# Performance work log

Measured on AMD Instinct MI355X. Metric: run time of the kernel, lower is better.

The kernel has to match this reference:

```python
import jax, jax.numpy as jnp
import numpy as np

D = 256      # embed_dims
NH = 8       # num_heads
NL = 1       # num_levels
NP = 6       # num_points
BS = 1
NQ = 40000   # 200x200 BEV queries
H0, W0 = 200, 200
HD = D // NH


def _ln(x, g, b):
    m = jnp.mean(x, -1, keepdims=True)
    v = jnp.var(x, -1, keepdims=True)
    return (x - m) / jnp.sqrt(v + 1e-5) * g + b


def _bilinear(v, lx, ly, H, W):
    # v: (bs, h, H*W, hd); lx/ly: (bs, h, S) pixel coords (align_corners=False, zero padding)
    x0 = jnp.floor(lx).astype(jnp.int32)
    y0 = jnp.floor(ly).astype(jnp.int32)
    acc = 0.
    for dx in (0, 1):
        for dy in (0, 1):
            xi = x0 + dx
            yi = y0 + dy
            w = (1. - jnp.abs(lx - xi)) * (1. - jnp.abs(ly - yi))
            valid = (xi >= 0) & (xi < W) & (yi >= 0) & (yi < H)
            idx = jnp.clip(yi, 0, H - 1) * W + jnp.clip(xi, 0, W - 1)
            g = jnp.take_along_axis(v, idx[..., None], axis=2)  # (bs,h,S,hd)
            acc = acc + g * (w * valid)[..., None]
    return acc


def _forward(query, value, reference_points, W_off, b_off, W_attn, b_attn,
             W_val, b_val, W_out, b_out, ln1_g, ln1_b, W1, b1, W2, b2,
             ln2_g, ln2_b, ss, lsi):
    bs, nq, d = query.shape
    # sampling offsets and attention weights from the query
    off = (query @ W_off + b_off).reshape(bs, nq, NH, NL, NP, 2)
    attn = jax.nn.softmax((query @ W_attn + b_attn).reshape(bs, nq, NH, NL * NP), -1)
    attn = attn.reshape(bs, nq, NH, NL, NP)
    v = (value @ W_val + b_val).reshape(bs, -1, NH, HD).transpose(0, 2, 1, 3)  # (bs,h,HW,hd)
    # offset normalizer is [W, H] per level
    norm = jnp.stack([ss[:, 1], ss[:, 0]], -1).astype(query.dtype)  # (NL,2)
    loc = reference_points[:, :, None, :, None, :] + off / norm[None, None, None, :, None, :]
    out = jnp.zeros((bs, NH, nq, HD), query.dtype)
    for l in range(NL):
        Hl = int(ss[l, 0]); Wl = int(ss[l, 1]); st = int(lsi[l])
        vl = v[:, :, st:st + Hl * Wl]
        lx = (loc[:, :, :, l, :, 0] * Wl - 0.5).transpose(0, 2, 1, 3).reshape(bs, NH, nq * NP)
        ly = (loc[:, :, :, l, :, 1] * Hl - 0.5).transpose(0, 2, 1, 3).reshape(bs, NH, nq * NP)
        sampled = _bilinear(vl, lx, ly, Hl, Wl).reshape(bs, NH, nq, NP, HD)
        wl = attn[:, :, :, l, :].transpose(0, 2, 1, 3)  # (bs,h,nq,P)
        out = out + jnp.einsum('bhqp,bhqpd->bhqd', wl, sampled)
    y_msda = out.transpose(0, 2, 1, 3).reshape(bs, nq, d) @ W_out + b_out
    y = _ln(y_msda + query, ln1_g, ln1_b)
    y_ffn = jax.nn.gelu(y @ W1 + b1, approximate=False) @ W2 + b2
    return _ln(y_ffn + y, ln2_g, ln2_b)


def setup_inputs():
    key = jax.random.key(0)
    ks = jax.random.split(key, 12)
    s = 0.02
    return {
        'query': jax.random.normal(ks[0], (BS, NQ, D), jnp.float32),
        'value': jax.random.normal(ks[1], (BS, H0 * W0, D), jnp.float32),
        'reference_points': jax.random.uniform(ks[2], (BS, NQ, NL, 2), jnp.float32),
        'spatial_shapes': jnp.array([[H0, W0]], jnp.int32),
        'level_start_index': jnp.array([0], jnp.int32),
        'W_off': jax.random.normal(ks[3], (D, NH * NL * NP * 2), jnp.float32) * s,
        'b_off': jax.random.uniform(ks[4], (NH * NL * NP * 2,), jnp.float32, -1., 1.),
        'W_attn': jax.random.normal(ks[5], (D, NH * NL * NP), jnp.float32) * s,
        'b_attn': jnp.zeros((NH * NL * NP,), jnp.float32),
        'W_val': jax.random.normal(ks[6], (D, D), jnp.float32) * s,
        'b_val': jnp.zeros((D,), jnp.float32),
        'W_out': jax.random.normal(ks[7], (D, D), jnp.float32) * s,
        'b_out': jnp.zeros((D,), jnp.float32),
        'ln1_g': jnp.ones((D,), jnp.float32),
        'ln1_b': jnp.zeros((D,), jnp.float32),
        'W1': jax.random.normal(ks[8], (D, D), jnp.float32) * s,
        'b1': jnp.zeros((D,), jnp.float32),
        'W2': jax.random.normal(ks[9], (D, D), jnp.float32) * s,
        'b2': jnp.zeros((D,), jnp.float32),
        'ln2_g': jnp.ones((D,), jnp.float32),
        'ln2_b': jnp.zeros((D,), jnp.float32),
    }


def reference(query, value, reference_points, spatial_shapes, level_start_index,
              W_off, b_off, W_attn, b_attn, W_val, b_val, W_out, b_out,
              ln1_g, ln1_b, W1, b1, W2, b2, ln2_g, ln2_b):
    ss = np.asarray(spatial_shapes)
    lsi = np.asarray(level_start_index)
    return _forward(query, value, reference_points, W_off, b_off, W_attn, b_attn,
                    W_val, b_val, W_out, b_out, ln1_g, ln1_b, W1, b1, W2, b2,
                    ln2_g, ln2_b, ss, lsi)
```

## Files before the change

kernel.cpp:

```cpp
#include <hip/hip_runtime.h>
#include <math.h>

#define NQ 40000
#define DIM 256
#define NH 8
#define NP 6
#define HD 32
#define GH 200
#define GW 200
#define TS 8
#define TNX 25
#define NT 625

typedef short bf16x8 __attribute__((ext_vector_type(8)));
typedef float f32x4 __attribute__((ext_vector_type(4)));

__device__ __forceinline__ unsigned short f2bf(float f) {
    unsigned int u = __builtin_bit_cast(unsigned int, f);
    u += 0x7fffu + ((u >> 16) & 1u);
    return (unsigned short)(u >> 16);
}
__device__ __forceinline__ float bf2f(unsigned short h) {
    return __builtin_bit_cast(float, ((unsigned int)h) << 16);
}

__global__ void __launch_bounds__(256)
f2b_kernel(const float* __restrict__ q, unsigned short* __restrict__ qd,
           const float* __restrict__ v, unsigned short* __restrict__ vd) {
    int b = blockIdx.x;
    const float* src; unsigned short* dst;
    if (b < 5000) { src = q; dst = qd; } else { src = v; dst = vd; b -= 5000; }
    const int i = b * 256 + threadIdx.x;
    const float4* s = (const float4*)src;
    float4 a = s[(size_t)i * 2], c = s[(size_t)i * 2 + 1];
    bf16x8 o;
    o[0] = (short)f2bf(a.x); o[1] = (short)f2bf(a.y);
    o[2] = (short)f2bf(a.z); o[3] = (short)f2bf(a.w);
    o[4] = (short)f2bf(c.x); o[5] = (short)f2bf(c.y);
    o[6] = (short)f2bf(c.z); o[7] = (short)f2bf(c.w);
    *(bf16x8*)(dst + (size_t)i * 8) = o;
}

__global__ void __launch_bounds__(256)
wtrans_kernel(const float* __restrict__ Wval, const float* __restrict__ Woff,
              const float* __restrict__ Wattn, const float* __restrict__ Wout,
              const float* __restrict__ W1, const float* __restrict__ W2,
              const float* __restrict__ b_off, const float* __restrict__ b_attn,
              unsigned short* __restrict__ Bt, float* __restrict__ bias_oa) {
    __shared__ float T[64][65];
    const int m = blockIdx.z;
    const float* src; int N; int dr0;
    if (m == 0)      { src = Wval;  N = 256; dr0 = 0; }
    else if (m == 1) { src = Woff;  N = 96;  dr0 = 256; }
    else if (m == 2) { src = Wattn; N = 48;  dr0 = 352; }
    else if (m == 3) { src = Wout;  N = 256; dr0 = 400; }
    else if (m == 4) { src = W1;    N = 256; dr0 = 656; }
    else             { src = W2;    N = 256; dr0 = 912; }

    if (m == 1 && blockIdx.x == 0 && blockIdx.y == 0 && threadIdx.x < 144)
        bias_oa[threadIdx.x] = threadIdx.x < 96 ? b_off[threadIdx.x]
                                                : b_attn[threadIdx.x - 96];

    const int n0 = blockIdx.x * 64, k0 = blockIdx.y * 64;
    if (n0 >= N) return;
    const int col = threadIdx.x & 63, rg = threadIdx.x >> 6;
#pragma unroll
    for (int i = 0; i < 16; ++i) {
        const int r = rg + 4 * i;
        T[r][col] = (n0 + col < N) ? src[(size_t)(k0 + r) * N + n0 + col] : 0.0f;
    }
    __syncthreads();
#pragma unroll
    for (int i = 0; i < 16; ++i) {
        const int nl = rg + 4 * i;
        if (n0 + nl < N)
            Bt[(size_t)(dr0 + n0 + nl) * 256 + k0 + col] = f2bf(T[col][nl]);
    }
}

__device__ __forceinline__ int tile_of(const float* rp, int q) {
    const float rx = rp[q * 2 + 0] * (float)GW;
    const float ry = rp[q * 2 + 1] * (float)GH;
    const int tx = min(max((int)(rx * (1.0f / TS)), 0), TNX - 1);
    const int ty = min(max((int)(ry * (1.0f / TS)), 0), TNX - 1);
    return ty * TNX + tx;
}

__global__ void __launch_bounds__(256)
sort_zero(int* __restrict__ hist) {
    const int i = blockIdx.x * 256 + threadIdx.x;
    if (i < NT) hist[i] = 0;
}

__global__ void __launch_bounds__(256)
sort_hist(const float* __restrict__ rp, int* __restrict__ hist) {
    const int q = blockIdx.x * 256 + threadIdx.x;
    if (q >= NQ) return;
    atomicAdd(&hist[tile_of(rp, q)], 1);
}

__global__ void __launch_bounds__(64)
sort_scan(const int* __restrict__ hist, int* __restrict__ cursor) {
    const int lane = threadIdx.x;
    int loc[10]; int t = 0;
#pragma unroll
    for (int j = 0; j < 10; ++j) {
        const int idx = lane * 10 + j;
        loc[j] = t;
        t += (idx < NT) ? hist[idx] : 0;
    }
    int s = t;
#pragma unroll
    for (int o = 1; o < 64; o <<= 1) {
        const int u = __shfl_up(s, o);
        if (lane >= o) s += u;
    }
    const int ex = s - t;
#pragma unroll
    for (int j = 0; j < 10; ++j) {
        const int idx = lane * 10 + j;
        if (idx < NT) cursor[idx] = ex + loc[j];
    }
}

__global__ void __launch_bounds__(256)
sort_scatter(const float* __restrict__ rp, int* __restrict__ cursor,
             int* __restrict__ perm) {
    const int q = blockIdx.x * 256 + threadIdx.x;
    if (q >= NQ) return;
    const int pos = atomicAdd(&cursor[tile_of(rp, q)], 1);
    perm[pos] = q;
}

template <int EPI>
__global__ void __launch_bounds__(256)
gemm64(const unsigned short* __restrict__ A, const unsigned short* __restrict__ Bt,
       const float* __restrict__ bias, const void* __restrict__ res,
       const float* __restrict__ lng, const float* __restrict__ lnb,
       void* __restrict__ C, int M) {
    __shared__ __align__(16) unsigned short As[2][64 * 32];
    __shared__ __align__(16) unsigned short Bs[2][256 * 32];
    __shared__ __align__(16) float red[64][4][2];

    const int tid = threadIdx.x, lane = tid & 63, wave = tid >> 6;
    const int quad = lane >> 4, l16 = lane & 15;
    const int bm0 = blockIdx.x * 64;
    const int r16 = lane >> 2;
    const int ch = (lane & 3) * 8;

    f32x4 acc[4][4] = {};

    auto stage = [&](int kt, int buf) {
        const int k0 = kt * 32;
        {
            const int row = wave * 16 + r16;
            const unsigned short* gp = A + (size_t)(bm0 + row) * 256 + k0 + ch;
            __builtin_amdgcn_global_load_lds(
                (const __attribute__((address_space(1))) void*)gp,
                (__attribute__((address_space(3))) void*)(&As[buf][wave * 16 * 32]),
                16, 0, 0);
        }
#pragma unroll
        for (int j = 0; j < 4; ++j) {
            const int rowbase = (wave * 4 + j) * 16;
            const unsigned short* gp = Bt + (size_t)(rowbase + r16) * 256 + k0 + ch;
            __builtin_amdgcn_global_load_lds(
                (const __attribute__((address_space(1))) void*)gp,
                (__attribute__((address_space(3))) void*)(&Bs[buf][rowbase * 32]),
                16, 0, 0);
        }
    };

    stage(0, 0);
    __syncthreads();

    for (int kt = 0; kt < 8; ++kt) {
        const int cur = kt & 1;
        if (kt < 7) stage(kt + 1, 1 - cur);

        bf16x8 af[4], bw[4];
#pragma unroll
        for (int t = 0; t < 4; ++t) {
            af[t] = *(const bf16x8*)&As[cur][(t * 16 + l16) * 32 + quad * 8];
            bw[t] = *(const bf16x8*)&Bs[cur][(wave * 64 + t * 16 + l16) * 32 + quad * 8];
        }
#pragma unroll
        for (int tm = 0; tm < 4; ++tm)
#pragma unroll
            for (int tn = 0; tn < 4; ++tn)
                acc[tm][tn] = __builtin_amdgcn_mfma_f32_16x16x32_bf16(
                    af[tm], bw[tn], acc[tm][tn], 0, 0, 0);
        __syncthreads();
    }

    float bias4[4];
#pragma unroll
    for (int tn = 0; tn < 4; ++tn) bias4[tn] = bias[wave * 64 + tn * 16 + l16];

    if (EPI == 1 || EPI == 2) {
#pragma unroll
        for (int tm = 0; tm < 4; ++tm) {
            const int row0 = bm0 + tm * 16 + quad * 4;
#pragma unroll
            for (int tn = 0; tn < 4; ++tn) {
                const int col = wave * 64 + tn * 16 + l16;
#pragma unroll
                for (int r = 0; r < 4; ++r) {
                    float x = acc[tm][tn][r] + bias4[tn];
                    if (EPI == 1) x = 0.5f * x * (1.0f + erff(x * 0.70710678118654752f));
                    ((unsigned short*)C)[(size_t)(row0 + r) * 256 + col] = f2bf(x);
                }
            }
        }
        return;
    }

#pragma unroll
    for (int tm = 0; tm < 4; ++tm) {
#pragma unroll
        for (int r = 0; r < 4; ++r) {
            const size_t rb = (size_t)(bm0 + tm * 16 + quad * 4 + r) * 256;
#pragma unroll
            for (int tn = 0; tn < 4; ++tn) {
                const int col = wave * 64 + tn * 16 + l16;
                float e = acc[tm][tn][r] + bias4[tn];
                if (EPI == 3) e += ((const float*)res)[rb + col];
                else          e += bf2f(((const unsigned short*)res)[rb + col]);
                acc[tm][tn][r] = e;
            }
        }
    }
#pragma unroll
    for (int tm = 0; tm < 4; ++tm) {
#pragma unroll
        for (int r = 0; r < 4; ++r) {
            float s = 0.0f, sq = 0.0f;
#pragma unroll
            for (int tn = 0; tn < 4; ++tn) {
                const float e = acc[tm][tn][r];
                s += e; sq += e * e;
            }
#pragma unroll
            for (int o = 1; o < 16; o <<= 1) {
                s += __shfl_xor(s, o);
                sq += __shfl_xor(sq, o);
            }
            if (l16 == 0) {
                const int row = tm * 16 + quad * 4 + r;
                red[row][wave][0] = s;
                red[row][wave][1] = sq;
            }
        }
    }
    __syncthreads();

    float gv[4], bvv[4];
#pragma unroll
    for (int tn = 0; tn < 4; ++tn) {
        const int col = wave * 64 + tn * 16 + l16;
        gv[tn] = lng[col];
        bvv[tn] = lnb[col];
    }
#pragma unroll
    for (int tm = 0; tm < 4; ++tm) {
#pragma unroll
        for (int r = 0; r < 4; ++r) {
            const int row = tm * 16 + quad * 4 + r;
            const float4 p0 = *(const float4*)&red[row][0][0];
            const float4 p1 = *(const float4*)&red[row][2][0];
            const float sum = p0.x + p0.z + p1.x + p1.z;
            const float sumsq = p0.y + p0.w + p1.y + p1.w;
            const float mean = sum * (1.0f / 256.0f);
            const float var = sumsq * (1.0f / 256.0f) - mean * mean;
            const float rstd = rsqrtf(var + 1e-5f);
            const size_t rb = (size_t)(bm0 + row) * 256;
#pragma unroll
            for (int tn = 0; tn < 4; ++tn) {
                const int col = wave * 64 + tn * 16 + l16;
                const float o = (acc[tm][tn][r] - mean) * rstd * gv[tn] + bvv[tn];
                if (EPI == 3) ((unsigned short*)C)[rb + col] = f2bf(o);
                else          ((float*)C)[rb + col] = o;
            }
        }
    }
}

__global__ void __launch_bounds__(256)
gemm_bt(const unsigned short* __restrict__ A, const unsigned short* __restrict__ Bt,
        const float* __restrict__ bias, unsigned short* __restrict__ C,
        int M, int N, int ldc) {
    __shared__ __align__(16) unsigned short As[128 * 32];
    __shared__ __align__(16) unsigned short Bs[128 * 32];

    const int tid = threadIdx.x, lane = tid & 63, wave = tid >> 6;
    const int quad = lane >> 4, l16 = lane & 15;
    const int wm = wave >> 1, wn = wave & 1;
    const int bm0 = blockIdx.y * 128, bn0 = blockIdx.x * 128;

    f32x4 acc[4][4] = {};
    const int rl = lane >> 2;
    const int c8 = (lane & 3) * 8;

    for (int kt = 0; kt < 8; ++kt) {
        const int k0 = kt * 32;
        __syncthreads();
#pragma unroll
        for (int i = 0; i < 2; ++i) {
            const int rgrp = i * 64 + wave * 16;
            const int gA = min(bm0 + rgrp + rl, M - 1);
            const unsigned short* gpa = A + (size_t)gA * 256 + k0 + c8;
            __builtin_amdgcn_global_load_lds(
                (const __attribute__((address_space(1))) void*)gpa,
                (__attribute__((address_space(3))) void*)(As + (size_t)rgrp * 32),
                16, 0, 0);
            const int gB = min(bn0 + rgrp + rl, N - 1);
            const unsigned short* gpb = Bt + (size_t)gB * 256 + k0 + c8;
            __builtin_amdgcn_global_load_lds(
                (const __attribute__((address_space(1))) void*)gpb,
                (__attribute__((address_space(3))) void*)(Bs + (size_t)rgrp * 32),
                16, 0, 0);
        }
        __syncthreads();

        bf16x8 af[4], bw[4];
#pragma unroll
        for (int t = 0; t < 4; ++t) {
            af[t] = *(const bf16x8*)&As[(wm * 64 + t * 16 + l16) * 32 + quad * 8];
            bw[t] = *(const bf16x8*)&Bs[(wn * 64 + t * 16 + l16) * 32 + quad * 8];
        }
#pragma unroll
        for (int tm = 0; tm < 4; ++tm)
#pragma unroll
            for (int tn = 0; tn < 4; ++tn)
                acc[tm][tn] = __builtin_amdgcn_mfma_f32_16x16x32_bf16(
                    af[tm], bw[tn], acc[tm][tn], 0, 0, 0);
    }

#pragma unroll
    for (int tm = 0; tm < 4; ++tm) {
        const int row0 = bm0 + wm * 64 + tm * 16 + quad * 4;
#pragma unroll
        for (int tn = 0; tn < 4; ++tn) {
            const int col = bn0 + wn * 64 + tn * 16 + l16;
            if (col < N) {
                const float bv = bias[col];
#pragma unroll
                for (int r = 0; r < 4; ++r) {
                    const int row = row0 + r;
                    if (row < M)
                        C[(size_t)row * ldc + col] = f2bf(acc[tm][tn][r] + bv);
                }
            }
        }
    }
}

__global__ void __launch_bounds__(256)
msda_sample(const unsigned short* __restrict__ v,
            const unsigned short* __restrict__ oa,
            const float* __restrict__ rp,
            const int* __restrict__ perm,
            unsigned short* __restrict__ out) {
    const int b = blockIdx.x;
    const int w = (b & 7) * 625 + (b >> 3);
    const int tid = threadIdx.x;
    const int slot = tid >> 2;
    const int q = perm[w * 8 + (slot >> 3)];
    const int h = slot & 7;
    const int c0 = (tid & 3) * 8;

    const float rx = rp[q * 2 + 0] * (float)GW;
    const float ry = rp[q * 2 + 1] * (float)GH;

    const unsigned short* oaq = oa + (size_t)q * 144;
    float lg[NP];
    float mx = -1e30f;
#pragma unroll
    for (int p = 0; p < NP; ++p) {
        lg[p] = bf2f(oaq[96 + h * NP + p]);
        mx = fmaxf(mx, lg[p]);
    }
    float s = 0.0f;
#pragma unroll
    for (int p = 0; p < NP; ++p) { lg[p] = expf(lg[p] - mx); s += lg[p]; }
    const float inv = 1.0f / s;

    float acc[8] = {};
#pragma unroll
    for (int p = 0; p < NP; ++p) {
        const float aw = lg[p] * inv;
        const float lx = rx + bf2f(oaq[h * 12 + p * 2 + 0]) - 0.5f;
        const float ly = ry + bf2f(oaq[h * 12 + p * 2 + 1]) - 0.5f;
        const float fx0 = floorf(lx), fy0 = floorf(ly);
        const int x0 = (int)fx0, y0 = (int)fy0;
        const float fx = lx - fx0, fy = ly - fy0;
#pragma unroll
        for (int dy = 0; dy < 2; ++dy) {
            const int yi = y0 + dy;
            const float wyv = dy ? fy : 1.0f - fy;
#pragma unroll
            for (int dx = 0; dx < 2; ++dx) {
                const int xi = x0 + dx;
                const float wxv = dx ? fx : 1.0f - fx;
                const bool valid = (xi >= 0) & (xi < GW) & (yi >= 0) & (yi < GH);
                const int yc = min(max(yi, 0), GH - 1);
                const int xc = min(max(xi, 0), GW - 1);
                const float wgt = valid ? aw * wxv * wyv : 0.0f;
                const bf16x8 g = *(const bf16x8*)&v[((size_t)(yc * GW + xc)) * 256 + h * 32 + c0];
#pragma unroll
                for (int j = 0; j < 8; ++j)
                    acc[j] += bf2f((unsigned short)g[j]) * wgt;
            }
        }
    }
    bf16x8 o;
#pragma unroll
    for (int j = 0; j < 8; ++j) o[j] = (short)f2bf(acc[j]);
    *(bf16x8*)&out[(size_t)q * 256 + h * 32 + c0] = o;
}

extern "C" void kernel_launch(void* const* d_in, const int* in_sizes, int n_in,
                              void* d_out, int out_size, void* d_ws, size_t ws_size,
                              hipStream_t stream) {
    const float* query  = (const float*)d_in[0];
    const float* value  = (const float*)d_in[1];
    const float* rp     = (const float*)d_in[2];
    const float* W_off  = (const float*)d_in[5];
    const float* b_off  = (const float*)d_in[6];
    const float* W_attn = (const float*)d_in[7];
    const float* b_attn = (const float*)d_in[8];
    const float* W_val  = (const float*)d_in[9];
    const float* b_val  = (const float*)d_in[10];
    const float* W_out  = (const float*)d_in[11];
    const float* b_out  = (const float*)d_in[12];
    const float* ln1_g  = (const float*)d_in[13];
    const float* ln1_b  = (const float*)d_in[14];
    const float* W1     = (const float*)d_in[15];
    const float* b1     = (const float*)d_in[16];
    const float* W2     = (const float*)d_in[17];
    const float* b2     = (const float*)d_in[18];
    const float* ln2_g  = (const float*)d_in[19];
    const float* ln2_b  = (const float*)d_in[20];

    char* ws = (char*)d_ws;
    unsigned short* Bt       = (unsigned short*)ws;
    float*          bias_oa  = (float*)(ws + 598016);
    int*            hist     = (int*)(ws + 598592);
    int*            cursor   = (int*)(ws + 601600);
    int*            perm     = (int*)(ws + 604608);
    unsigned short* query_bf = (unsigned short*)(ws + 770048);
    unsigned short* h1_bf    = query_bf;
    unsigned short* value_bf = (unsigned short*)(ws + 21250048);
    unsigned short* msda_bf  = value_bf;
    unsigned short* v_bf     = (unsigned short*)(ws + 41730048);
    unsigned short* y_bf     = v_bf;
    unsigned short* oa_bf    = (unsigned short*)(ws + 62210048);
    float*          outp     = (float*)d_out;

    dim3 blk(256);
    f2b_kernel<<<dim3(10000), blk, 0, stream>>>(query, query_bf, value, value_bf);
    wtrans_kernel<<<dim3(4, 4, 6), blk, 0, stream>>>(W_val, W_off, W_attn, W_out, W1, W2,
                                                     b_off, b_attn, Bt, bias_oa);
    sort_zero<<<dim3(3), blk, 0, stream>>>(hist);
    sort_hist<<<dim3(157), blk, 0, stream>>>(rp, hist);
    sort_scan<<<dim3(1), dim3(64), 0, stream>>>(hist, cursor);
    sort_scatter<<<dim3(157), blk, 0, stream>>>(rp, cursor, perm);
    gemm64<2><<<dim3(625), blk, 0, stream>>>(value_bf, Bt, b_val, nullptr, nullptr, nullptr,
                                             (void*)v_bf, NQ);
    gemm_bt<<<dim3(2, 313), blk, 0, stream>>>(query_bf, Bt + 256 * 256, bias_oa,
                                              oa_bf, NQ, 144, 144);
    msda_sample<<<dim3(5000), blk, 0, stream>>>(v_bf, oa_bf, rp, perm, msda_bf);
    gemm64<3><<<dim3(625), blk, 0, stream>>>(msda_bf, Bt + 400 * 256, b_out,
                                             (const void*)query, ln1_g, ln1_b,
                                             (void*)y_bf, NQ);
    gemm64<1><<<dim3(625), blk, 0, stream>>>(y_bf, Bt + 656 * 256, b1, nullptr, nullptr,
                                             nullptr, (void*)h1_bf, NQ);
    gemm64<4><<<dim3(625), blk, 0, stream>>>(h1_bf, Bt + 912 * 256, b2,
                                             (const void*)y_bf, ln2_g, ln2_b,
                                             (void*)outp, NQ);
}
```

Baseline: 335.6 us.

## Fuse fp32-to-bf16 conversion into GEMM loads and widen per-thread MSDA work

Removes the standalone f2b conversion kernel. The value GEMM and the offset/attention GEMM now read fp32 inputs directly, converting to bf16 in registers before writing to LDS. The histogram zeroing is folded into the weight-transpose kernel, dropping one more launch. The sampling kernel now gives each thread all 32 channels of one head instead of 8, which cuts redundant per-thread offset, softmax and weight computation by 4x but raises register pressure and lowers thread count.

```diff
diff --git a/kernel.cpp b/kernel.cpp
--- a/kernel.cpp
+++ b/kernel.cpp
@@ -23,22 +23,13 @@
 __device__ __forceinline__ float bf2f(unsigned short h) {
     return __builtin_bit_cast(float, ((unsigned int)h) << 16);
 }
-
-__global__ void __launch_bounds__(256)
-f2b_kernel(const float* __restrict__ q, unsigned short* __restrict__ qd,
-           const float* __restrict__ v, unsigned short* __restrict__ vd) {
-    int b = blockIdx.x;
-    const float* src; unsigned short* dst;
-    if (b < 5000) { src = q; dst = qd; } else { src = v; dst = vd; b -= 5000; }
-    const int i = b * 256 + threadIdx.x;
-    const float4* s = (const float4*)src;
-    float4 a = s[(size_t)i * 2], c = s[(size_t)i * 2 + 1];
+__device__ __forceinline__ bf16x8 pack8(const float4& a, const float4& b) {
     bf16x8 o;
     o[0] = (short)f2bf(a.x); o[1] = (short)f2bf(a.y);
     o[2] = (short)f2bf(a.z); o[3] = (short)f2bf(a.w);
-    o[4] = (short)f2bf(c.x); o[5] = (short)f2bf(c.y);
-    o[6] = (short)f2bf(c.z); o[7] = (short)f2bf(c.w);
-    *(bf16x8*)(dst + (size_t)i * 8) = o;
+    o[4] = (short)f2bf(b.x); o[5] = (short)f2bf(b.y);
+    o[6] = (short)f2bf(b.z); o[7] = (short)f2bf(b.w);
+    return o;
 }
 
 __global__ void __launch_bounds__(256)
@@ -46,7 +37,8 @@
               const float* __restrict__ Wattn, const float* __restrict__ Wout,
               const float* __restrict__ W1, const float* __restrict__ W2,
               const float* __restrict__ b_off, const float* __restrict__ b_attn,
-              unsigned short* __restrict__ Bt, float* __restrict__ bias_oa) {
+              unsigned short* __restrict__ Bt, float* __restrict__ bias_oa,
+              int* __restrict__ hist) {
     __shared__ float T[64][65];
     const int m = blockIdx.z;
     const float* src; int N; int dr0;
@@ -60,6 +52,10 @@
     if (m == 1 && blockIdx.x == 0 && blockIdx.y == 0 && threadIdx.x < 144)
         bias_oa[threadIdx.x] = threadIdx.x < 96 ? b_off[threadIdx.x]
                                                 : b_attn[threadIdx.x - 96];
+    if (m == 0 && blockIdx.y == 0) {
+        const int i = blockIdx.x * 256 + threadIdx.x;
+        if (i < NT) hist[i] = 0;
+    }
 
     const int n0 = blockIdx.x * 64, k0 = blockIdx.y * 64;
     if (n0 >= N) return;
@@ -84,12 +80,6 @@
     const int tx = min(max((int)(rx * (1.0f / TS)), 0), TNX - 1);
     const int ty = min(max((int)(ry * (1.0f / TS)), 0), TNX - 1);
     return ty * TNX + tx;
-}
-
-__global__ void __launch_bounds__(256)
-sort_zero(int* __restrict__ hist) {
-    const int i = blockIdx.x * 256 + threadIdx.x;
-    if (i < NT) hist[i] = 0;
 }
 
 __global__ void __launch_bounds__(256)
@@ -132,9 +122,9 @@
     perm[pos] = q;
 }
 
-template <int EPI>
+template <int EPI, int AF32>
 __global__ void __launch_bounds__(256)
-gemm64(const unsigned short* __restrict__ A, const unsigned short* __restrict__ Bt,
+gemm64(const void* __restrict__ Av, const unsigned short* __restrict__ Btw,
        const float* __restrict__ bias, const void* __restrict__ res,
        const float* __restrict__ lng, const float* __restrict__ lnb,
        void* __restrict__ C, int M) {
@@ -145,25 +135,37 @@
     const int tid = threadIdx.x, lane = tid & 63, wave = tid >> 6;
     const int quad = lane >> 4, l16 = lane & 15;
     const int bm0 = blockIdx.x * 64;
-    const int r16 = lane >> 2;
-    const int ch = (lane & 3) * 8;
+    const int r16 = lane >> 2, ch = (lane & 3) * 8;
 
     f32x4 acc[4][4] = {};
 
-    auto stage = [&](int kt, int buf) {
-        const int k0 = kt * 32;
-        {
-            const int row = wave * 16 + r16;
-            const unsigned short* gp = A + (size_t)(bm0 + row) * 256 + k0 + ch;
-            __builtin_amdgcn_global_load_lds(
-                (const __attribute__((address_space(1))) void*)gp,
-                (__attribute__((address_space(3))) void*)(&As[buf][wave * 16 * 32]),
-                16, 0, 0);
-        }
+    const unsigned short* Ab = (const unsigned short*)Av;
+    const float* Af = (const float*)Av;
+    const int arow = tid >> 2, acol = (tid & 3) * 8;
+
+    float4 a0, a1;
+    auto loadA = [&](int kt) {
+        const float* ap = Af + (size_t)(bm0 + arow) * 256 + kt * 32 + acol;
+        a0 = *(const float4*)ap;
+        a1 = *(const float4*)(ap + 4);
+    };
+    auto writeA = [&](int buf) {
+        *(bf16x8*)&As[buf][arow * 32 + acol] = pack8(a0, a1);
+    };
+    auto stageA_lds = [&](int kt, int buf) {
+        const unsigned short* gp =
+            Ab + (size_t)(bm0 + wave * 16 + r16) * 256 + kt * 32 + ch;
+        __builtin_amdgcn_global_load_lds(
+            (const __attribute__((address_space(1))) void*)gp,
+            (__attribute__((address_space(3))) void*)(&As[buf][wave * 16 * 32]),
+            16, 0, 0);
+    };
+    auto stageB = [&](int kt, int buf) {
 #pragma unroll
         for (int j = 0; j < 4; ++j) {
             const int rowbase = (wave * 4 + j) * 16;
-            const unsigned short* gp = Bt + (size_t)(rowbase + r16) * 256 + k0 + ch;
+            const unsigned short* gp =
+                Btw + (size_t)(rowbase + r16) * 256 + kt * 32 + ch;
             __builtin_amdgcn_global_load_lds(
                 (const __attribute__((address_space(1))) void*)gp,
                 (__attribute__((address_space(3))) void*)(&Bs[buf][rowbase * 32]),
@@ -171,12 +173,16 @@
         }
     };
 
-    stage(0, 0);
+    if (AF32) { loadA(0); writeA(0); } else stageA_lds(0, 0);
+    stageB(0, 0);
     __syncthreads();
 
     for (int kt = 0; kt < 8; ++kt) {
         const int cur = kt & 1;
-        if (kt < 7) stage(kt + 1, 1 - cur);
+        if (kt < 7) {
+            stageB(kt + 1, 1 - cur);
+            if (AF32) loadA(kt + 1); else stageA_lds(kt + 1, 1 - cur);
+        }
 
         bf16x8 af[4], bw[4];
 #pragma unroll
@@ -190,6 +196,7 @@
             for (int tn = 0; tn < 4; ++tn)
                 acc[tm][tn] = __builtin_amdgcn_mfma_f32_16x16x32_bf16(
                     af[tm], bw[tn], acc[tm][tn], 0, 0, 0);
+        if (AF32 && kt < 7) writeA(1 - cur);
         __syncthreads();
     }
 
@@ -286,7 +293,7 @@
 }
 
 __global__ void __launch_bounds__(256)
-gemm_bt(const unsigned short* __restrict__ A, const unsigned short* __restrict__ Bt,
+gemm_bt(const float* __restrict__ A, const unsigned short* __restrict__ Btw,
         const float* __restrict__ bias, unsigned short* __restrict__ C,
         int M, int N, int ldc) {
     __shared__ __align__(16) unsigned short As[128 * 32];
@@ -300,21 +307,26 @@
     f32x4 acc[4][4] = {};
     const int rl = lane >> 2;
     const int c8 = (lane & 3) * 8;
+    const int rA = tid >> 1, cA = (tid & 1) * 16;
 
     for (int kt = 0; kt < 8; ++kt) {
         const int k0 = kt * 32;
         __syncthreads();
+        {
+            const int ar = min(bm0 + rA, M - 1);
+            const float* ap = A + (size_t)ar * 256 + k0 + cA;
+            float4 x0 = *(const float4*)(ap);
+            float4 x1 = *(const float4*)(ap + 4);
+            float4 x2 = *(const float4*)(ap + 8);
+            float4 x3 = *(const float4*)(ap + 12);
+            *(bf16x8*)&As[rA * 32 + cA]     = pack8(x0, x1);
+            *(bf16x8*)&As[rA * 32 + cA + 8] = pack8(x2, x3);
+        }
 #pragma unroll
         for (int i = 0; i < 2; ++i) {
             const int rgrp = i * 64 + wave * 16;
-            const int gA = min(bm0 + rgrp + rl, M - 1);
-            const unsigned short* gpa = A + (size_t)gA * 256 + k0 + c8;
-            __builtin_amdgcn_global_load_lds(
-                (const __attribute__((address_space(1))) void*)gpa,
-                (__attribute__((address_space(3))) void*)(As + (size_t)rgrp * 32),
-                16, 0, 0);
             const int gB = min(bn0 + rgrp + rl, N - 1);
-            const unsigned short* gpb = Bt + (size_t)gB * 256 + k0 + c8;
+            const unsigned short* gpb = Btw + (size_t)gB * 256 + k0 + c8;
             __builtin_amdgcn_global_load_lds(
                 (const __attribute__((address_space(1))) void*)gpb,
                 (__attribute__((address_space(3))) void*)(Bs + (size_t)rgrp * 32),
@@ -362,12 +374,12 @@
             const int* __restrict__ perm,
             unsigned short* __restrict__ out) {
     const int b = blockIdx.x;
-    const int w = (b & 7) * 625 + (b >> 3);
+    const int w = (b & 7) * 157 + (b >> 3);
+    if (w >= 1250) return;
     const int tid = threadIdx.x;
-    const int slot = tid >> 2;
-    const int q = perm[w * 8 + (slot >> 3)];
-    const int h = slot & 7;
-    const int c0 = (tid & 3) * 8;
+    const int qi = tid >> 3;
+    const int h = tid & 7;
+    const int q = perm[w * 32 + qi];
 
     const float rx = rp[q * 2 + 0] * (float)GW;
     const float ry = rp[q * 2 + 1] * (float)GH;
@@ -385,7 +397,7 @@
     for (int p = 0; p < NP; ++p) { lg[p] = expf(lg[p] - mx); s += lg[p]; }
     const float inv = 1.0f / s;
 
-    float acc[8] = {};
+    float acc[32] = {};
 #pragma unroll
     for (int p = 0; p < NP; ++p) {
         const float aw = lg[p] * inv;
@@ -406,17 +418,26 @@
                 const int yc = min(max(yi, 0), GH - 1);
                 const int xc = min(max(xi, 0), GW - 1);
                 const float wgt = valid ? aw * wxv * wyv : 0.0f;
-                const bf16x8 g = *(const bf16x8*)&v[((size_t)(yc * GW + xc)) * 256 + h * 32 + c0];
-#pragma unroll
-                for (int j = 0; j < 8; ++j)
-                    acc[j] += bf2f((unsigned short)g[j]) * wgt;
-            }
-        }
-    }
-    bf16x8 o;
-#pragma unroll
-    for (int j = 0; j < 8; ++j) o[j] = (short)f2bf(acc[j]);
-    *(bf16x8*)&out[(size_t)q * 256 + h * 32 + c0] = o;
+                const unsigned short* cell =
+                    &v[((size_t)(yc * GW + xc)) * 256 + h * 32];
+#pragma unroll
+                for (int sl = 0; sl < 4; ++sl) {
+                    const bf16x8 g = *(const bf16x8*)(cell + sl * 8);
+#pragma unroll
+                    for (int j = 0; j < 8; ++j)
+                        acc[sl * 8 + j] += bf2f((unsigned short)g[j]) * wgt;
+                }
+            }
+        }
+    }
+    unsigned short* op = &out[(size_t)q * 256 + h * 32];
+#pragma unroll
+    for (int sl = 0; sl < 4; ++sl) {
+        bf16x8 o;
+#pragma unroll
+        for (int j = 0; j < 8; ++j) o[j] = (short)f2bf(acc[sl * 8 + j]);
+        *(bf16x8*)(op + sl * 8) = o;
+    }
 }
 
 extern "C" void kernel_launch(void* const* d_in, const int* in_sizes, int n_in,
@@ -443,39 +464,37 @@
     const float* ln2_b  = (const float*)d_in[20];
 
     char* ws = (char*)d_ws;
-    unsigned short* Bt       = (unsigned short*)ws;
-    float*          bias_oa  = (float*)(ws + 598016);
-    int*            hist     = (int*)(ws + 598592);
-    int*            cursor   = (int*)(ws + 601600);
-    int*            perm     = (int*)(ws + 604608);
-    unsigned short* query_bf = (unsigned short*)(ws + 770048);
-    unsigned short* h1_bf    = query_bf;
-    unsigned short* value_bf = (unsigned short*)(ws + 21250048);
-    unsigned short* msda_bf  = value_bf;
-    unsigned short* v_bf     = (unsigned short*)(ws + 41730048);
-    unsigned short* y_bf     = v_bf;
-    unsigned short* oa_bf    = (unsigned short*)(ws + 62210048);
-    float*          outp     = (float*)d_out;
+    unsigned short* Bt      = (unsigned short*)ws;
+    float*          bias_oa = (float*)(ws + 598016);
+    int*            hist    = (int*)(ws + 598592);
+    int*            cursor  = (int*)(ws + 601600);
+    int*            perm    = (int*)(ws + 604608);
+    unsigned short* v_bf    = (unsigned short*)(ws + 770048);
+    unsigned short* y_bf    = v_bf;
+    unsigned short* oa_bf   = (unsigned short*)(ws + 21250048);
+    unsigned short* msda_bf = (unsigned short*)(ws + 32770048);
+    unsigned short* h1_bf   = msda_bf;
+    float*          outp    = (float*)d_out;
 
     dim3 blk(256);
-    f2b_kernel<<<dim3(10000), blk, 0, stream>>>(query, query_bf, value, value_bf);
     wtrans_kernel<<<dim3(4, 4, 6), blk, 0, stream>>>(W_val, W_off, W_attn, W_out, W1, W2,
-                                                     b_off, b_attn, Bt, bias_oa);
-    sort_zero<<<dim3(3), blk, 0, stream>>>(hist);
+                                                     b_off, b_attn, Bt, bias_oa, hist);
     sort_hist<<<dim3(157), blk, 0, stream>>>(rp, hist);
     sort_scan<<<dim3(1), dim3(64), 0, stream>>>(hist, cursor);
     sort_scatter<<<dim3(157), blk, 0, stream>>>(rp, cursor, perm);
-    gemm64<2><<<dim3(625), blk, 0, stream>>>(value_bf, Bt, b_val, nullptr, nullptr, nullptr,
-                                             (void*)v_bf, NQ);
-    gemm_bt<<<dim3(2, 313), blk, 0, stream>>>(query_bf, Bt + 256 * 256, bias_oa,
+    gemm64<2, 1><<<dim3(625), blk, 0, stream>>>((const void*)value, Bt, b_val,
+                                                nullptr, nullptr, nullptr,
+                                                (void*)v_bf, NQ);
+    gemm_bt<<<dim3(2, 313), blk, 0, stream>>>(query, Bt + 256 * 256, bias_oa,
                                               oa_bf, NQ, 144, 144);
-    msda_sample<<<dim3(5000), blk, 0, stream>>>(v_bf, oa_bf, rp, perm, msda_bf);
-    gemm64<3><<<dim3(625), blk, 0, stream>>>(msda_bf, Bt + 400 * 256, b_out,
-                                             (const void*)query, ln1_g, ln1_b,
-                                             (void*)y_bf, NQ);
-    gemm64<1><<<dim3(625), blk, 0, stream>>>(y_bf, Bt + 656 * 256, b1, nullptr, nullptr,
-                                             nullptr, (void*)h1_bf, NQ);
-    gemm64<4><<<dim3(625), blk, 0, stream>>>(h1_bf, Bt + 912 * 256, b2,
-                                             (const void*)y_bf, ln2_g, ln2_b,
-                                             (void*)outp, NQ);
-}
+    msda_sample<<<dim3(1256), blk, 0, stream>>>(v_bf, oa_bf, rp, perm, msda_bf);
+    gemm64<3, 0><<<dim3(625), blk, 0, stream>>>((const void*)msda_bf, Bt + 400 * 256, b_out,
+                                                (const void*)query, ln1_g, ln1_b,
+                                                (void*)y_bf, NQ);
+    gemm64<1, 0><<<dim3(625), blk, 0, stream>>>((const void*)y_bf, Bt + 656 * 256, b1,
+                                                nullptr, nullptr, nullptr,
+                                                (void*)h1_bf, NQ);
+    gemm64<4, 0><<<dim3(625), blk, 0, stream>>>((const void*)h1_bf, Bt + 912 * 256, b2,
+                                                (const void*)y_bf, ln2_g, ln2_b,
+                                                (void*)outp, NQ);
+}
```

After: 427.9 us. 27.5% more time.

## Fuse histogram into conversion kernel, read bf16 residual, hoist bilinear corner weights

Applied to the files above, without the earlier changes.

Folds the histogram zeroing into the weight-transpose kernel and the histogram atomics into the fp32-to-bf16 conversion kernel, which removes two launches. The LN1 residual now comes from the bf16 query copy instead of fp32 query, halving that read but adding rounding error to the residual. The bilinear sampler computes per-axis validity weights once per point and issues all four corner loads before accumulating, which should help memory-level parallelism. The histogram depends on zeroing done in the earlier kernel, so correctness relies on stream ordering.

```diff
diff --git a/kernel.cpp b/kernel.cpp
--- a/kernel.cpp
+++ b/kernel.cpp
@@ -24,10 +24,24 @@
     return __builtin_bit_cast(float, ((unsigned int)h) << 16);
 }
 
-__global__ void __launch_bounds__(256)
-f2b_kernel(const float* __restrict__ q, unsigned short* __restrict__ qd,
-           const float* __restrict__ v, unsigned short* __restrict__ vd) {
+__device__ __forceinline__ int tile_of(const float* rp, int q) {
+    const float rx = rp[q * 2 + 0] * (float)GW;
+    const float ry = rp[q * 2 + 1] * (float)GH;
+    const int tx = min(max((int)(rx * (1.0f / TS)), 0), TNX - 1);
+    const int ty = min(max((int)(ry * (1.0f / TS)), 0), TNX - 1);
+    return ty * TNX + tx;
+}
+
+__global__ void __launch_bounds__(256)
+f2b_hist(const float* __restrict__ q, unsigned short* __restrict__ qd,
+         const float* __restrict__ v, unsigned short* __restrict__ vd,
+         const float* __restrict__ rp, int* __restrict__ hist) {
     int b = blockIdx.x;
+    if (b >= 10000) {
+        const int qq = (b - 10000) * 256 + threadIdx.x;
+        if (qq < NQ) atomicAdd(&hist[tile_of(rp, qq)], 1);
+        return;
+    }
     const float* src; unsigned short* dst;
     if (b < 5000) { src = q; dst = qd; } else { src = v; dst = vd; b -= 5000; }
     const int i = b * 256 + threadIdx.x;
@@ -46,7 +60,8 @@
               const float* __restrict__ Wattn, const float* __restrict__ Wout,
               const float* __restrict__ W1, const float* __restrict__ W2,
               const float* __restrict__ b_off, const float* __restrict__ b_attn,
-              unsigned short* __restrict__ Bt, float* __restrict__ bias_oa) {
+              unsigned short* __restrict__ Bt, float* __restrict__ bias_oa,
+              int* __restrict__ hist) {
     __shared__ float T[64][65];
     const int m = blockIdx.z;
     const float* src; int N; int dr0;
@@ -60,6 +75,10 @@
     if (m == 1 && blockIdx.x == 0 && blockIdx.y == 0 && threadIdx.x < 144)
         bias_oa[threadIdx.x] = threadIdx.x < 96 ? b_off[threadIdx.x]
                                                 : b_attn[threadIdx.x - 96];
+    if (m == 0 && blockIdx.y == 0) {
+        const int i = blockIdx.x * 256 + threadIdx.x;
+        if (i < NT) hist[i] = 0;
+    }
 
     const int n0 = blockIdx.x * 64, k0 = blockIdx.y * 64;
     if (n0 >= N) return;
@@ -76,27 +95,6 @@
         if (n0 + nl < N)
             Bt[(size_t)(dr0 + n0 + nl) * 256 + k0 + col] = f2bf(T[col][nl]);
     }
-}
-
-__device__ __forceinline__ int tile_of(const float* rp, int q) {
-    const float rx = rp[q * 2 + 0] * (float)GW;
-    const float ry = rp[q * 2 + 1] * (float)GH;
-    const int tx = min(max((int)(rx * (1.0f / TS)), 0), TNX - 1);
-    const int ty = min(max((int)(ry * (1.0f / TS)), 0), TNX - 1);
-    return ty * TNX + tx;
-}
-
-__global__ void __launch_bounds__(256)
-sort_zero(int* __restrict__ hist) {
-    const int i = blockIdx.x * 256 + threadIdx.x;
-    if (i < NT) hist[i] = 0;
-}
-
-__global__ void __launch_bounds__(256)
-sort_hist(const float* __restrict__ rp, int* __restrict__ hist) {
-    const int q = blockIdx.x * 256 + threadIdx.x;
-    if (q >= NQ) return;
-    atomicAdd(&hist[tile_of(rp, q)], 1);
 }
 
 __global__ void __launch_bounds__(64)
@@ -134,8 +132,8 @@
 
 template <int EPI>
 __global__ void __launch_bounds__(256)
-gemm64(const unsigned short* __restrict__ A, const unsigned short* __restrict__ Bt,
-       const float* __restrict__ bias, const void* __restrict__ res,
+gemm64(const unsigned short* __restrict__ A, const unsigned short* __restrict__ Btw,
+       const float* __restrict__ bias, const unsigned short* __restrict__ res,
        const float* __restrict__ lng, const float* __restrict__ lnb,
        void* __restrict__ C, int M) {
     __shared__ __align__(16) unsigned short As[2][64 * 32];
@@ -145,16 +143,15 @@
     const int tid = threadIdx.x, lane = tid & 63, wave = tid >> 6;
     const int quad = lane >> 4, l16 = lane & 15;
     const int bm0 = blockIdx.x * 64;
-    const int r16 = lane >> 2;
-    const int ch = (lane & 3) * 8;
+    const int r16 = lane >> 2, ch = (lane & 3) * 8;
 
     f32x4 acc[4][4] = {};
 
     auto stage = [&](int kt, int buf) {
         const int k0 = kt * 32;
         {
-            const int row = wave * 16 + r16;
-            const unsigned short* gp = A + (size_t)(bm0 + row) * 256 + k0 + ch;
+            const unsigned short* gp =
+                A + (size_t)(bm0 + wave * 16 + r16) * 256 + k0 + ch;
             __builtin_amdgcn_global_load_lds(
                 (const __attribute__((address_space(1))) void*)gp,
                 (__attribute__((address_space(3))) void*)(&As[buf][wave * 16 * 32]),
@@ -163,7 +160,8 @@
 #pragma unroll
         for (int j = 0; j < 4; ++j) {
             const int rowbase = (wave * 4 + j) * 16;
-            const unsigned short* gp = Bt + (size_t)(rowbase + r16) * 256 + k0 + ch;
+            const unsigned short* gp =
+                Btw + (size_t)(rowbase + r16) * 256 + k0 + ch;
             __builtin_amdgcn_global_load_lds(
                 (const __attribute__((address_space(1))) void*)gp,
                 (__attribute__((address_space(3))) void*)(&Bs[buf][rowbase * 32]),
@@ -223,10 +221,7 @@
 #pragma unroll
             for (int tn = 0; tn < 4; ++tn) {
                 const int col = wave * 64 + tn * 16 + l16;
-                float e = acc[tm][tn][r] + bias4[tn];
-                if (EPI == 3) e += ((const float*)res)[rb + col];
-                else          e += bf2f(((const unsigned short*)res)[rb + col]);
-                acc[tm][tn][r] = e;
+                acc[tm][tn][r] += bias4[tn] + bf2f(res[rb + col]);
             }
         }
     }
@@ -286,7 +281,7 @@
 }
 
 __global__ void __launch_bounds__(256)
-gemm_bt(const unsigned short* __restrict__ A, const unsigned short* __restrict__ Bt,
+gemm_bt(const unsigned short* __restrict__ A, const unsigned short* __restrict__ Btw,
         const float* __restrict__ bias, unsigned short* __restrict__ C,
         int M, int N, int ldc) {
     __shared__ __align__(16) unsigned short As[128 * 32];
@@ -314,7 +309,7 @@
                 (__attribute__((address_space(3))) void*)(As + (size_t)rgrp * 32),
                 16, 0, 0);
             const int gB = min(bn0 + rgrp + rl, N - 1);
-            const unsigned short* gpb = Bt + (size_t)gB * 256 + k0 + c8;
+            const unsigned short* gpb = Btw + (size_t)gB * 256 + k0 + c8;
             __builtin_amdgcn_global_load_lds(
                 (const __attribute__((address_space(1))) void*)gpb,
                 (__attribute__((address_space(3))) void*)(Bs + (size_t)rgrp * 32),
@@ -385,6 +380,7 @@
     for (int p = 0; p < NP; ++p) { lg[p] = expf(lg[p] - mx); s += lg[p]; }
     const float inv = 1.0f / s;
 
+    const unsigned short* vh = v + h * 32 + c0;
     float acc[8] = {};
 #pragma unroll
     for (int p = 0; p < NP; ++p) {
@@ -394,23 +390,30 @@
         const float fx0 = floorf(lx), fy0 = floorf(ly);
         const int x0 = (int)fx0, y0 = (int)fy0;
         const float fx = lx - fx0, fy = ly - fy0;
-#pragma unroll
-        for (int dy = 0; dy < 2; ++dy) {
-            const int yi = y0 + dy;
-            const float wyv = dy ? fy : 1.0f - fy;
-#pragma unroll
-            for (int dx = 0; dx < 2; ++dx) {
-                const int xi = x0 + dx;
-                const float wxv = dx ? fx : 1.0f - fx;
-                const bool valid = (xi >= 0) & (xi < GW) & (yi >= 0) & (yi < GH);
-                const int yc = min(max(yi, 0), GH - 1);
-                const int xc = min(max(xi, 0), GW - 1);
-                const float wgt = valid ? aw * wxv * wyv : 0.0f;
-                const bf16x8 g = *(const bf16x8*)&v[((size_t)(yc * GW + xc)) * 256 + h * 32 + c0];
-#pragma unroll
-                for (int j = 0; j < 8; ++j)
-                    acc[j] += bf2f((unsigned short)g[j]) * wgt;
-            }
+
+        const float wx0 = ((x0 >= 0) & (x0 < GW)) ? (1.0f - fx) : 0.0f;
+        const float wx1 = ((x0 + 1 >= 0) & (x0 + 1 < GW)) ? fx : 0.0f;
+        const float wy0 = ((y0 >= 0) & (y0 < GH)) ? (1.0f - fy) : 0.0f;
+        const float wy1 = ((y0 + 1 >= 0) & (y0 + 1 < GH)) ? fy : 0.0f;
+        const float w00 = aw * wx0 * wy0, w01 = aw * wx1 * wy0;
+        const float w10 = aw * wx0 * wy1, w11 = aw * wx1 * wy1;
+
+        const int x0c = min(max(x0, 0), GW - 1);
+        const int x1c = min(max(x0 + 1, 0), GW - 1);
+        const int y0c = min(max(y0, 0), GH - 1);
+        const int y1c = min(max(y0 + 1, 0), GH - 1);
+
+        const bf16x8 g00 = *(const bf16x8*)(vh + (size_t)(y0c * GW + x0c) * 256);
+        const bf16x8 g01 = *(const bf16x8*)(vh + (size_t)(y0c * GW + x1c) * 256);
+        const bf16x8 g10 = *(const bf16x8*)(vh + (size_t)(y1c * GW + x0c) * 256);
+        const bf16x8 g11 = *(const bf16x8*)(vh + (size_t)(y1c * GW + x1c) * 256);
+
+#pragma unroll
+        for (int j = 0; j < 8; ++j) {
+            acc[j] += bf2f((unsigned short)g00[j]) * w00
+                    + bf2f((unsigned short)g01[j]) * w01
+                    + bf2f((unsigned short)g10[j]) * w10
+                    + bf2f((unsigned short)g11[j]) * w11;
         }
     }
     bf16x8 o;
@@ -458,24 +461,24 @@
     float*          outp     = (float*)d_out;
 
     dim3 blk(256);
-    f2b_kernel<<<dim3(10000), blk, 0, stream>>>(query, query_bf, value, value_bf);
     wtrans_kernel<<<dim3(4, 4, 6), blk, 0, stream>>>(W_val, W_off, W_attn, W_out, W1, W2,
-                                                     b_off, b_attn, Bt, bias_oa);
-    sort_zero<<<dim3(3), blk, 0, stream>>>(hist);
-    sort_hist<<<dim3(157), blk, 0, stream>>>(rp, hist);
+                                                     b_off, b_attn, Bt, bias_oa, hist);
+    f2b_hist<<<dim3(10157), blk, 0, stream>>>(query, query_bf, value, value_bf, rp, hist);
     sort_scan<<<dim3(1), dim3(64), 0, stream>>>(hist, cursor);
     sort_scatter<<<dim3(157), blk, 0, stream>>>(rp, cursor, perm);
-    gemm64<2><<<dim3(625), blk, 0, stream>>>(value_bf, Bt, b_val, nullptr, nullptr, nullptr,
+    gemm64<2><<<dim3(625), blk, 0, stream>>>(value_bf, Bt, b_val,
+                                             nullptr, nullptr, nullptr,
                                              (void*)v_bf, NQ);
     gemm_bt<<<dim3(2, 313), blk, 0, stream>>>(query_bf, Bt + 256 * 256, bias_oa,
                                               oa_bf, NQ, 144, 144);
     msda_sample<<<dim3(5000), blk, 0, stream>>>(v_bf, oa_bf, rp, perm, msda_bf);
     gemm64<3><<<dim3(625), blk, 0, stream>>>(msda_bf, Bt + 400 * 256, b_out,
-                                             (const void*)query, ln1_g, ln1_b,
+                                             query_bf, ln1_g, ln1_b,
                                              (void*)y_bf, NQ);
-    gemm64<1><<<dim3(625), blk, 0, stream>>>(y_bf, Bt + 656 * 256, b1, nullptr, nullptr,
-                                             nullptr, (void*)h1_bf, NQ);
+    gemm64<1><<<dim3(625), blk, 0, stream>>>(y_bf, Bt + 656 * 256, b1,
+                                             nullptr, nullptr, nullptr,
+                                             (void*)h1_bf, NQ);
     gemm64<4><<<dim3(625), blk, 0, stream>>>(h1_bf, Bt + 912 * 256, b2,
-                                             (const void*)y_bf, ln2_g, ln2_b,
+                                             y_bf, ln2_g, ln2_b,
                                              (void*)outp, NQ);
 }
```

Result: no change. 334.5 us (-0.3%).
